# Optimization experiments

Measured on AMD Instinct MI355X. Metric: run time of the kernel, lower is better.

## Reference

```python
import jax, jax.numpy as jnp
import numpy as np

B, S, D, H = 2, 2048, 1024, 16
DH = D // H  # 64


def setup_inputs() -> dict:
    key = jax.random.key(0)
    ks = jax.random.split(key, 12)
    scale = 0.02
    q = jax.random.normal(ks[0], (B, S, D), dtype=jnp.float32)
    k = jax.random.normal(ks[1], (B, S, D), dtype=jnp.float32)
    v = jax.random.normal(ks[2], (B, S, D), dtype=jnp.float32)
    # CTRL-style causal mask: 1.0 above the diagonal (positions to mask), 0.0 elsewhere
    mask = jnp.triu(jnp.ones((S, S), dtype=jnp.float32), k=1)
    Wq = jax.random.normal(ks[3], (D, D), dtype=jnp.float32) * scale
    bq = jnp.zeros((D,), dtype=jnp.float32)
    Wk = jax.random.normal(ks[4], (D, D), dtype=jnp.float32) * scale
    bk = jnp.zeros((D,), dtype=jnp.float32)
    Wv = jax.random.normal(ks[5], (D, D), dtype=jnp.float32) * scale
    bv = jnp.zeros((D,), dtype=jnp.float32)
    Wo = jax.random.normal(ks[6], (D, D), dtype=jnp.float32) * scale
    bo = jnp.zeros((D,), dtype=jnp.float32)
    return {"q": q, "k": k, "v": v, "mask": mask,
            "Wq": Wq, "bq": bq, "Wk": Wk, "bk": bk,
            "Wv": Wv, "bv": bv, "Wo": Wo, "bo": bo}


def _split_heads(x):
    # [B, S, D] -> [B, H, S, DH]
    b, s, _ = x.shape
    return x.reshape(b, s, H, DH).transpose(0, 2, 1, 3)


def reference(q, k, v, mask, Wq, bq, Wk, bk, Wv, bv, Wo, bo):
    # QKV projections
    qh = _split_heads(q @ Wq + bq)  # [B, H, S, DH]
    kh = _split_heads(k @ Wk + bk)
    vh = _split_heads(v @ Wv + bv)
    # scaled dot-product attention with CTRL mask convention (mask * -1e4 added)
    scores = jnp.einsum('bhqd,bhkd->bhqk', qh, kh) / jnp.sqrt(jnp.float32(DH))
    scores = scores + mask * -10000.0  # mask broadcasts [S,S] -> [B,H,S,S]
    weights = jax.nn.softmax(scores, axis=-1)
    ctx = jnp.einsum('bhqk,bhkd->bhqd', weights, vh)  # [B, H, S, DH]
    ctx = ctx.transpose(0, 2, 1, 3).reshape(q.shape[0], -1, D)  # [B, S, D]
    return ctx @ Wo + bo
```

## Files before the change

### kernel.cpp

```cpp
#include <hip/hip_runtime.h>
#include <stdint.h>

typedef unsigned short u16;
typedef __attribute__((ext_vector_type(8))) short bf16x8;
typedef __attribute__((ext_vector_type(4))) float f32x4;
typedef __attribute__((ext_vector_type(4))) unsigned short u16x4;

#define C_SCALE 0.1803368801111204f
#define C_MASK  -14426.950408889634f

__device__ __forceinline__ float bf2f(u16 x) {
  union { uint32_t u; float f; } v; v.u = ((uint32_t)x) << 16; return v.f;
}
__device__ __forceinline__ u16 f2bf(float f) {
  union { float f; uint32_t u; } v; v.f = f;
  return (u16)((v.u + 0x7FFFu + ((v.u >> 16) & 1u)) >> 16);
}

__device__ __forceinline__ void load_lds16(const void* g, void* l) {
  __builtin_amdgcn_global_load_lds(
      (const __attribute__((address_space(1))) uint32_t*)g,
      (__attribute__((address_space(3))) uint32_t*)l, 16, 0, 0);
}

__device__ __forceinline__ uint32_t pack_trunc(uint32_t f_even, uint32_t f_odd) {
  return __builtin_amdgcn_perm(f_odd, f_even, 0x07060302u);
}

__device__ __forceinline__ uint32_t cvtpk_bf16(float lo, float hi) {
  uint32_t r;
  asm("v_cvt_pk_bf16_f32 %0, %1, %2" : "=v"(r) : "v"(lo), "v"(hi));
  return r;
}

__device__ __forceinline__ bool detect_bf16(const u16* __restrict__ q) {
  int lane = threadIdx.x & 63;
  u16 w = q[lane * 4];
  int e = (w >> 7) & 0xFF;
  unsigned long long b = __ballot(e >= 96 && e <= 159);
  return __popcll(b) >= 48;
}

__global__ __launch_bounds__(256) void prep_all(const u16* __restrict__ W0,
                                                const u16* __restrict__ W1,
                                                const u16* __restrict__ W2,
                                                const u16* __restrict__ W3,
                                                u16* __restrict__ WTb,
                                                const u16* __restrict__ q,
                                                const u16* __restrict__ k,
                                                const u16* __restrict__ v,
                                                u16* __restrict__ Acast,
                                                int docast) {
  constexpr int D = 1024;
  const int z = blockIdx.z;
  const bool isbf = detect_bf16(q);

  if (z >= 4) {
    if (!docast || isbf) return;
    const int zi = z - 4;
    const u16* src = zi == 0 ? q : (zi == 1 ? k : v);
    const uint32_t* S = (const uint32_t*)src;
    u16* dst = Acast + (size_t)zi * 4 * 1024 * 1024;
    const int fb = blockIdx.y * 16 + blockIdx.x;
    const int t = threadIdx.x;
#pragma unroll
    for (int it = 0; it < 8; ++it) {
      size_t base = (size_t)fb * 16384 + it * 2048 + t * 8;
      uint4 a = *(const uint4*)&S[base];
      uint4 b = *(const uint4*)&S[base + 4];
      uint4 o;
      o.x = pack_trunc(a.x, a.y); o.y = pack_trunc(a.z, a.w);
      o.z = pack_trunc(b.x, b.y); o.w = pack_trunc(b.z, b.w);
      *(uint4*)&dst[base] = o;
    }
    return;
  }

  __shared__ u16 tile[64][72];
  const u16* W = z == 0 ? W0 : (z == 1 ? W1 : (z == 2 ? W2 : W3));
  u16* WT = WTb + (size_t)z * D * D;
  const int x0 = blockIdx.x * 64, y0 = blockIdx.y * 64;
  const int t = threadIdx.x;
  const int r = t >> 3;
  const int c8 = (t & 7) << 3;
#pragma unroll
  for (int hh = 0; hh < 2; ++hh) {
    int row = r + hh * 32;
    if (isbf) {
      *(uint4*)&tile[row][c8] = *(const uint4*)&W[(size_t)(y0 + row) * D + x0 + c8];
    } else {
      const float* Wf = (const float*)W;
      float4 f0 = *(const float4*)&Wf[(size_t)(y0 + row) * D + x0 + c8];
      float4 f1 = *(const float4*)&Wf[(size_t)(y0 + row) * D + x0 + c8 + 4];
      u16 tmp[8] = {f2bf(f0.x), f2bf(f0.y), f2bf(f0.z), f2bf(f0.w),
                    f2bf(f1.x), f2bf(f1.y), f2bf(f1.z), f2bf(f1.w)};
      *(uint4*)&tile[row][c8] = *(uint4*)tmp;
    }
  }
  __syncthreads();
#pragma unroll
  for (int hh = 0; hh < 2; ++hh) {
    int row = r + hh * 32;
    u16 tmp[8];
#pragma unroll
    for (int i = 0; i < 8; ++i) tmp[i] = tile[c8 + i][row];
    *(uint4*)&WT[(size_t)(x0 + row) * D + y0 + c8] = *(uint4*)tmp;
  }
}


__device__ __forceinline__ void stage_tile32(const u16* __restrict__ src, int row0,
                                             int k0, u16* dst, int wave, int lane) {
  constexpr int K = 1024;
#pragma unroll
  for (int p = 0; p < 2; ++p) {
    int seg = wave * 2 + p;
    int r = seg * 16 + (lane >> 2);
    int c = lane & 3;
    int cg = c ^ ((r >> 1) & 3);
    load_lds16(&src[(size_t)(row0 + r) * K + k0 + cg * 8], dst + seg * 512);
  }
}

#define FRAG_READS(Ab, Bb)                                                    \
  _Pragma("unroll") for (int i = 0; i < 4; ++i) {                             \
    int r = wm + 16 * i + lr;                                                 \
    af[i] = *(const bf16x8*)&(Ab)[r * 32 + ((quad ^ ((r >> 1) & 3)) * 8)];    \
  }                                                                           \
  _Pragma("unroll") for (int jj = 0; jj < 4; ++jj) {                          \
    int r = wn + 16 * jj + lr;                                                \
    bff[jj] = *(const bf16x8*)&(Bb)[r * 32 + ((quad ^ ((r >> 1) & 3)) * 8)];  \
  }

#define MFMA16()                                                              \
  _Pragma("unroll") for (int i = 0; i < 4; ++i)                               \
  _Pragma("unroll") for (int jj = 0; jj < 4; ++jj)                            \
      acc[i][jj] = __builtin_amdgcn_mfma_f32_16x16x32_bf16(af[i], bff[jj],    \
                                                           acc[i][jj], 0, 0, 0);

__device__ __forceinline__ void kloop2_dma(const u16* __restrict__ A,
                                           const u16* __restrict__ BT,
                                           int m0, int n0, u16* As, u16* Bs,
                                           int wave, int lane, f32x4 (&acc)[4][4]) {
  const int quad = lane >> 4, lr = lane & 15;
  const int wm = (wave & 1) * 64, wn = (wave >> 1) * 64;
  auto stage = [&](int t, int buf) {
    stage_tile32(A, m0, t * 32, As + buf * 4096, wave, lane);
    stage_tile32(BT, n0, t * 32, Bs + buf * 4096, wave, lane);
  };
  stage(0, 0);
  __syncthreads();
#pragma unroll 1
  for (int j = 0; j < 16; ++j) {
    const int t0 = 2 * j;
    {
      stage(t0 + 1, 1);
      bf16x8 af[4], bff[4];
      const u16 *Ab = As, *Bb = Bs;
      FRAG_READS(Ab, Bb)
      MFMA16()
      __syncthreads();
    }
    {
      if (t0 + 2 < 32) stage(t0 + 2, 0);
      bf16x8 af[4], bff[4];
      const u16 *Ab = As + 4096, *Bb = Bs + 4096;
      FRAG_READS(Ab, Bb)
      MFMA16()
      __syncthreads();
    }
  }
}

__device__ __forceinline__ void kloop2_f32(const float* __restrict__ Af,
                                           const u16* __restrict__ BT,
                                           int m0, int n0, u16* As, u16* Bs,
                                           int tid, f32x4 (&acc)[4][4]) {
  constexpr int K = 1024;
  const int wave = tid >> 6, lane = tid & 63;
  const int quad = lane >> 4, lr = lane & 15;
  const int wm = (wave & 1) * 64, wn = (wave >> 1) * 64;
  const int ar = tid >> 1, ah = tid & 1;
  const uint32_t* Au = (const uint32_t*)Af;
  uint4 ra0[4], ra1[4];
  auto loadA = [&](int t, uint4 (&r)[4]) {
    const uint32_t* p = &Au[(size_t)(m0 + ar) * K + t * 32 + ah * 16];
    r[0] = *(const uint4*)(p + 0);
    r[1] = *(const uint4*)(p + 4);
    r[2] = *(const uint4*)(p + 8);
    r[3] = *(const uint4*)(p + 12);
  };
  auto writeA = [&](int buf, uint4 (&rr)[4]) {
    uint4 o0, o1;
    o0.x = pack_trunc(rr[0].x, rr[0].y); o0.y = pack_trunc(rr[0].z, rr[0].w);
    o0.z = pack_trunc(rr[1].x, rr[1].y); o0.w = pack_trunc(rr[1].z, rr[1].w);
    o1.x = pack_trunc(rr[2].x, rr[2].y); o1.y = pack_trunc(rr[2].z, rr[2].w);
    o1.z = pack_trunc(rr[3].x, rr[3].y); o1.w = pack_trunc(rr[3].z, rr[3].w);
    int sw = (ar >> 1) & 3;
    int c0 = (2 * ah) ^ sw, c1 = (2 * ah + 1) ^ sw;
    *(uint4*)&As[buf * 4096 + ar * 32 + c0 * 8] = o0;
    *(uint4*)&As[buf * 4096 + ar * 32 + c1 * 8] = o1;
  };
  auto stageB = [&](int t, int buf) {
    stage_tile32(BT, n0, t * 32, Bs + buf * 4096, wave, lane);
  };
  loadA(0, ra0);
  stageB(0, 0);
  loadA(1, ra1);
  writeA(0, ra0);
  __syncthreads();
#pragma unroll 1
  for (int j = 0; j < 16; ++j) {
    const int t0 = 2 * j;
    {
      stageB(t0 + 1, 1);
      writeA(1, ra1);
      if (t0 + 2 < 32) loadA(t0 + 2, ra0);
      bf16x8 af[4], bff[4];
      const u16 *Ab = As, *Bb = Bs;
      FRAG_READS(Ab, Bb)
      MFMA16()
      __syncthreads();
    }
    {
      if (t0 + 2 < 32) { stageB(t0 + 2, 0); writeA(0, ra0); }
      if (t0 + 3 < 32) loadA(t0 + 3, ra1);
      bf16x8 af[4], bff[4];
      const u16 *Ab = As + 4096, *Bb = Bs + 4096;
      FRAG_READS(Ab, Bb)
      MFMA16()
      __syncthreads();
    }
  }
}

__device__ __forceinline__ void qkv_epilogue(int z, int n0, int m0, int wn, int wm,
                                             int quad, int lr, const u16* bias,
                                             bool isbf, f32x4 (&acc)[4][4],
                                             u16* __restrict__ C) {
  const float osc = (z == 0) ? C_SCALE : 1.0f;
#pragma unroll
  for (int i = 0; i < 4; ++i) {
#pragma unroll
    for (int jj = 0; jj < 4; ++jj) {
      int n = n0 + wn + 16 * jj + lr;
      float bv = isbf ? bf2f(bias[n]) : ((const float*)bias)[n];
#pragma unroll
      for (int r = 0; r < 4; ++r) {
        int m = m0 + wm + 16 * i + quad * 4 + r;
        float val = (acc[i][jj][r] + bv) * osc;
        int b = m >> 11, s = m & 2047, h = n >> 6, dh = n & 63;
        size_t idx;
        if (z == 2) idx = ((size_t)(b * 16 + h) * 64 + dh) * 2048 + s;
        else        idx = ((size_t)(b * 16 + h) * 2048 + s) * 64 + dh;
        C[idx] = f2bf(val);
      }
    }
  }
}

__global__ __launch_bounds__(256, 3) void gemm_qkv_pre(
    const u16* __restrict__ q, const u16* __restrict__ k, const u16* __restrict__ v,
    const u16* __restrict__ Acast, const u16* __restrict__ WTb,
    const u16* __restrict__ b0, const u16* __restrict__ b1, const u16* __restrict__ b2,
    u16* __restrict__ Chb) {
  __shared__ u16 As[2 * 4096];
  __shared__ u16 Bs[2 * 4096];
  const int z = blockIdx.y;
  const bool isbf = detect_bf16(q);
  const u16* Araw = z == 0 ? q : (z == 1 ? k : v);
  const u16* A = isbf ? Araw : Acast + (size_t)z * 4 * 1024 * 1024;
  const u16* bias = z == 0 ? b0 : (z == 1 ? b1 : b2);
  const u16* BT = WTb + (size_t)z * 1024 * 1024;
  u16* C = Chb + (size_t)z * 4 * 1024 * 1024;
  const int tid = threadIdx.x;
  const int wave = tid >> 6, lane = tid & 63;
  const int quad = lane >> 4, lr = lane & 15;
  const int f = blockIdx.x;
  const int n0 = (f >> 5) * 128;
  const int m0 = (f & 31) * 128;
  const int wm = (wave & 1) * 64, wn = (wave >> 1) * 64;

  f32x4 acc[4][4] = {};
  kloop2_dma(A, BT, m0, n0, As, Bs, wave, lane, acc);
  qkv_epilogue(z, n0, m0, wn, wm, quad, lr, bias, isbf, acc, C);
}

__global__ __launch_bounds__(256, 3) void gemm_qkv_fb(
    const u16* __restrict__ A0, const u16* __restrict__ A1, const u16* __restrict__ A2,
    const u16* __restrict__ WTb,
    const u16* __restrict__ b0, const u16* __restrict__ b1, const u16* __restrict__ b2,
    u16* __restrict__ Chb) {
  __shared__ u16 As[2 * 4096];
  __shared__ u16 Bs[2 * 4096];
  const int z = blockIdx.y;
  const u16* A = z == 0 ? A0 : (z == 1 ? A1 : A2);
  const u16* bias = z == 0 ? b0 : (z == 1 ? b1 : b2);
  const u16* BT = WTb + (size_t)z * 1024 * 1024;
  u16* C = Chb + (size_t)z * 4 * 1024 * 1024;
  const bool isbf = detect_bf16(A0);
  const int tid = threadIdx.x;
  const int wave = tid >> 6, lane = tid & 63;
  const int quad = lane >> 4, lr = lane & 15;
  const int f = blockIdx.x;
  const int n0 = (f >> 5) * 128;
  const int m0 = (f & 31) * 128;
  const int wm = (wave & 1) * 64, wn = (wave >> 1) * 64;

  f32x4 acc[4][4] = {};
  if (isbf) kloop2_dma(A, BT, m0, n0, As, Bs, wave, lane, acc);
  else      kloop2_f32((const float*)A, BT, m0, n0, As, Bs, tid, acc);
  qkv_epilogue(z, n0, m0, wn, wm, quad, lr, bias, isbf, acc, C);
}

__global__ __launch_bounds__(256, 2) void gemm_out(const u16* __restrict__ A,
                                                   const u16* __restrict__ BT,
                                                   const u16* __restrict__ bias,
                                                   u16* __restrict__ C,
                                                   const u16* __restrict__ qprobe) {
  constexpr int N = 1024, K = 1024;
  __shared__ u16 As[2 * 2048];
  __shared__ u16 Bs[2 * 4096];
  const bool isbf = detect_bf16(qprobe);
  const int tid = threadIdx.x;
  const int wave = tid >> 6, lane = tid & 63;
  const int quad = lane >> 4, lr = lane & 15;
  const int f = blockIdx.x;
  const int n0 = (f >> 6) * 128;
  const int m0 = (f & 63) * 64;
  const int wm = (wave & 1) * 32, wn = (wave >> 1) * 64;

  auto stage = [&](int t, int buf) {
    {
      int r = wave * 16 + (lane >> 2);
      int c = lane & 3;
      int cg = c ^ ((r >> 1) & 3);
      load_lds16(&A[(size_t)(m0 + r) * K + t * 32 + cg * 8],
                 As + buf * 2048 + wave * 512);
    }
    stage_tile32(BT, n0, t * 32, Bs + buf * 4096, wave, lane);
  };

  f32x4 acc[2][4] = {};
  stage(0, 0);
  __syncthreads();
#pragma unroll 1
  for (int j = 0; j < 16; ++j) {
    const int t0 = 2 * j;
#pragma unroll
    for (int half = 0; half < 2; ++half) {
      const int t = t0 + half;
      if (t + 1 < 32) stage(t + 1, (t + 1) & 1);
      bf16x8 af[2], bff[4];
      const u16* Ab = As + (t & 1) * 2048;
      const u16* Bb = Bs + (t & 1) * 4096;
#pragma unroll
      for (int i = 0; i < 2; ++i) {
        int r = wm + 16 * i + lr;
        af[i] = *(const bf16x8*)&Ab[r * 32 + ((quad ^ ((r >> 1) & 3)) * 8)];
      }
#pragma unroll
      for (int jj = 0; jj < 4; ++jj) {
        int r = wn + 16 * jj + lr;
        bff[jj] = *(const bf16x8*)&Bb[r * 32 + ((quad ^ ((r >> 1) & 3)) * 8)];
      }
#pragma unroll
      for (int i = 0; i < 2; ++i)
#pragma unroll
        for (int jj = 0; jj < 4; ++jj)
          acc[i][jj] =
              __builtin_amdgcn_mfma_f32_16x16x32_bf16(af[i], bff[jj], acc[i][jj], 0, 0, 0);
      __syncthreads();
    }
  }

#pragma unroll
  for (int i = 0; i < 2; ++i) {
#pragma unroll
    for (int jj = 0; jj < 4; ++jj) {
      int n = n0 + wn + 16 * jj + lr;
      float bv = isbf ? bf2f(bias[n]) : ((const float*)bias)[n];
#pragma unroll
      for (int r = 0; r < 4; ++r) {
        int m = m0 + wm + 16 * i + quad * 4 + r;
        float val = acc[i][jj][r] + bv;
        size_t idx = (size_t)m * N + n;
        if (isbf) C[idx] = f2bf(val);
        else ((float*)C)[idx] = val;
      }
    }
  }
}

__global__ __launch_bounds__(256, 2) void attn_fwd(const u16* __restrict__ Qh,
                                                   const u16* __restrict__ Kh,
                                                   const u16* __restrict__ VTh,
                                                   u16* __restrict__ ctx) {
  constexpr int S = 2048, DH = 64, Dm = 1024;
  __shared__ u16 Ks[2][64 * 64];
  __shared__ u16 Vs[2][64 * 64];
  __shared__ u16 Pl[4][16 * 72];
  const int tid = threadIdx.x;
  const int wave = tid >> 6, lane = tid & 63;
  const int quad = lane >> 4, lr = lane & 15;
  const int bh = blockIdx.y;
  const int bx = (int)blockIdx.x;
  const u16* Q  = Qh  + (size_t)bh * S * DH;
  const u16* Kp = Kh  + (size_t)bh * S * DH;
  const u16* Vt = VTh + (size_t)bh * S * DH;
  u16* Plw = Pl[wave];
  const int b = bh >> 4, h = bh & 15;

  auto stageK = [&](int kt, int kbuf) {
#pragma unroll
    for (int p = 0; p < 2; ++p) {
      int s = (wave * 2 + p) * 64 + lane;
      int r = s >> 3, cg = (s & 7) ^ (r & 7);
      load_lds16(&Kp[(size_t)(kt + r) * DH + cg * 8], &Ks[kbuf][(wave * 2 + p) * 512]);
    }
  };
  auto stageV = [&](int kt, int vbuf) {
#pragma unroll
    for (int p = 0; p < 2; ++p) {
      int s = (wave * 2 + p) * 64 + lane;
      int r = s >> 3, cg = (s & 7) ^ (r & 7);
      load_lds16(&Vt[(size_t)r * S + kt + cg * 8], &Vs[vbuf][(wave * 2 + p) * 512]);
    }
  };

  int kb = 0, vb = 0;
  for (int ph = 0; ph < 2; ++ph) {
    const int qt = ph == 0 ? (31 - bx) : bx;
    const int q0 = qt * 64;
    const int nt = qt + 1;
    const int qg = q0 + wave * 16 + lr;

    bf16x8 aQ[2];
#pragma unroll
    for (int s = 0; s < 2; ++s)
      aQ[s] = *(const bf16x8*)&Q[(size_t)(q0 + wave * 16 + lr) * DH + s * 32 + quad * 8];

    f32x4 o[4] = {};
    float m_i = -1.0e5f;
    float l_i = 0.f;

    __syncthreads();
    stageK(0, kb);
    stageV(0, vb);

    for (int it = 0; it < nt; ++it) {
      const int kt = it * 64;
      __syncthreads();

      bf16x8 aK[4][2], bV[4][2];
#pragma unroll
      for (int t = 0; t < 4; ++t) {
        int r = t * 16 + lr;
#pragma unroll
        for (int s = 0; s < 2; ++s) {
          int ch = (s * 4 + quad) ^ (r & 7);
          aK[t][s] = *(const bf16x8*)&Ks[kb][r * 64 + ch * 8];
        }
      }
#pragma unroll
      for (int c = 0; c < 4; ++c) {
        int rr = c * 16 + lr;
#pragma unroll
        for (int s = 0; s < 2; ++s) {
          int ch = (s * 4 + quad) ^ (rr & 7);
          bV[c][s] = *(const bf16x8*)&Vs[vb][rr * 64 + ch * 8];
        }
      }

      if (it + 1 < nt) {
        stageK(kt + 64, kb ^ 1);
        stageV(kt + 64, vb ^ 1);
      }

      f32x4 sc[4];
#pragma unroll
      for (int t = 0; t < 4; ++t) {
        f32x4 zz = {0.f, 0.f, 0.f, 0.f};
        zz = __builtin_amdgcn_mfma_f32_16x16x32_bf16(aK[t][0], aQ[0], zz, 0, 0, 0);
        zz = __builtin_amdgcn_mfma_f32_16x16x32_bf16(aK[t][1], aQ[1], zz, 0, 0, 0);
        sc[t] = zz;
      }

      const bool diag = (it == nt - 1);
      float v[4][4];
      float mx = -1.0e5f;
      if (diag) {
#pragma unroll
        for (int t = 0; t < 4; ++t)
#pragma unroll
          for (int r = 0; r < 4; ++r) {
            int kg = kt + t * 16 + quad * 4 + r;
            float x = sc[t][r] + ((kg > qg) ? C_MASK : 0.f);
            v[t][r] = x;
            mx = fmaxf(mx, x);
          }
      } else {
#pragma unroll
        for (int t = 0; t < 4; ++t)
#pragma unroll
          for (int r = 0; r < 4; ++r) {
            float x = sc[t][r];
            v[t][r] = x;
            mx = fmaxf(mx, x);
          }
      }
      mx = fmaxf(mx, __shfl_xor(mx, 16));
      mx = fmaxf(mx, __shfl_xor(mx, 32));

      const bool noresc = __all(mx <= m_i + 8.0f);
      const float m_new = noresc ? m_i : fmaxf(m_i, mx);

      float sum = 0.f;
      uint32_t pw[4][2];
#pragma unroll
      for (int t = 0; t < 4; ++t) {
        float p0 = exp2f(v[t][0] - m_new);
        float p1 = exp2f(v[t][1] - m_new);
        float p2 = exp2f(v[t][2] - m_new);
        float p3 = exp2f(v[t][3] - m_new);
        sum += p0 + p1 + p2 + p3;
        pw[t][0] = cvtpk_bf16(p0, p1);
        pw[t][1] = cvtpk_bf16(p2, p3);
      }
      sum += __shfl_xor(sum, 16);
      sum += __shfl_xor(sum, 32);

      if (noresc) {
        l_i += sum;
      } else {
        float alpha = exp2f(m_i - m_new);
        l_i = l_i * alpha + sum;
        m_i = m_new;
#pragma unroll
        for (int r = 0; r < 4; ++r) {
          float ab = __shfl(alpha, quad * 4 + r);
#pragma unroll
          for (int c = 0; c < 4; ++c) o[c][r] *= ab;
        }
      }
#pragma unroll
      for (int t = 0; t < 4; ++t) {
        uint2 w = {pw[t][0], pw[t][1]};
        *(uint2*)&Plw[lr * 72 + t * 16 + quad * 4] = w;
      }
      asm volatile("s_waitcnt lgkmcnt(0)" ::: "memory");
      bf16x8 aP[2];
#pragma unroll
      for (int s = 0; s < 2; ++s)
        aP[s] = *(const bf16x8*)&Plw[lr * 72 + s * 32 + quad * 8];
#pragma unroll
      for (int c = 0; c < 4; ++c)
#pragma unroll
        for (int s = 0; s < 2; ++s)
          o[c] = __builtin_amdgcn_mfma_f32_16x16x32_bf16(aP[s], bV[c][s], o[c], 0, 0, 0);
      kb ^= 1; vb ^= 1;
    }

    float linv = 1.f / l_i;
#pragma unroll
    for (int r = 0; r < 4; ++r) {
      float lb = __shfl(linv, quad * 4 + r);
      int s = q0 + wave * 16 + quad * 4 + r;
      size_t orow = ((size_t)b * S + s) * Dm + h * DH;
#pragma unroll
      for (int c = 0; c < 4; ++c) ctx[orow + c * 16 + lr] = f2bf(o[c][r] * lb);
    }
  }
}

extern "C" void kernel_launch(void* const* d_in, const int* in_sizes, int n_in,
                              void* d_out, int out_size, void* d_ws, size_t ws_size,
                              hipStream_t stream) {
  const u16* q  = (const u16*)d_in[0];
  const u16* k  = (const u16*)d_in[1];
  const u16* v  = (const u16*)d_in[2];
  const u16* Wq = (const u16*)d_in[4];
  const u16* bq = (const u16*)d_in[5];
  const u16* Wk = (const u16*)d_in[6];
  const u16* bk = (const u16*)d_in[7];
  const u16* Wv = (const u16*)d_in[8];
  const u16* bv = (const u16*)d_in[9];
  const u16* Wo = (const u16*)d_in[10];
  const u16* bo = (const u16*)d_in[11];
  u16* out = (u16*)d_out;

  constexpr size_t M1 = 1024 * 1024;
  u16* ws = (u16*)d_ws;
  u16* WT  = ws;
  u16* Qh  = WT + 4 * M1;
  u16* X   = Qh + 12 * M1;
  u16* Acast = X;
  u16* ctx   = X;

  const bool docast = ws_size >= (size_t)28 * M1 * 2;

  dim3 tb(256);
  prep_all<<<dim3(16, 16, 7), tb, 0, stream>>>(Wq, Wk, Wv, Wo, WT, q, k, v,
                                               Acast, docast ? 1 : 0);
  if (docast)
    gemm_qkv_pre<<<dim3(256, 3), tb, 0, stream>>>(q, k, v, Acast, WT, bq, bk, bv, Qh);
  else
    gemm_qkv_fb<<<dim3(256, 3), tb, 0, stream>>>(q, k, v, WT, bq, bk, bv, Qh);
  attn_fwd<<<dim3(16, 32), tb, 0, stream>>>(Qh, Qh + 4 * M1, Qh + 8 * M1, ctx);
  gemm_out<<<dim3(512), tb, 0, stream>>>(ctx, WT + 3 * M1, bo, out, q);
}
```

Baseline: 233.0 us.

## Fuse paired causal query tiles into one K/V sweep sharing staged tiles

The attention kernel used to process its two query tiles (31-bx and bx) in two sequential passes, each streaming K/V from the start. It now runs a single sweep over key tiles up to the larger tile's diagonal, with both query tiles consuming each staged K/V tile. The small tile is updated only while it <= bx, and each tile has its own P scratch buffer in LDS. This removes about bx+1 redundant K/V stage loads and one pipeline restart per block, at the cost of more registers (two accumulator sets) and larger LDS use, which could reduce occupancy.

```diff
diff --git a/kernel.cpp b/kernel.cpp
--- a/kernel.cpp
+++ b/kernel.cpp
@@ -399,7 +399,7 @@
   constexpr int S = 2048, DH = 64, Dm = 1024;
   __shared__ u16 Ks[2][64 * 64];
   __shared__ u16 Vs[2][64 * 64];
-  __shared__ u16 Pl[4][16 * 72];
+  __shared__ u16 Pl[4][2][16 * 72];
   const int tid = threadIdx.x;
   const int wave = tid >> 6, lane = tid & 63;
   const int quad = lane >> 4, lr = lane & 15;
@@ -408,8 +408,9 @@
   const u16* Q  = Qh  + (size_t)bh * S * DH;
   const u16* Kp = Kh  + (size_t)bh * S * DH;
   const u16* Vt = VTh + (size_t)bh * S * DH;
-  u16* Plw = Pl[wave];
   const int b = bh >> 4, h = bh & 15;
+  u16* PlA = Pl[wave][0];
+  u16* PlB = Pl[wave][1];
 
   auto stageK = [&](int kt, int kbuf) {
 #pragma unroll
@@ -428,74 +429,86 @@
     }
   };
 
-  int kb = 0, vb = 0;
-  for (int ph = 0; ph < 2; ++ph) {
-    const int qt = ph == 0 ? (31 - bx) : bx;
-    const int q0 = qt * 64;
-    const int nt = qt + 1;
-    const int qg = q0 + wave * 16 + lr;
-
-    bf16x8 aQ[2];
-#pragma unroll
-    for (int s = 0; s < 2; ++s)
-      aQ[s] = *(const bf16x8*)&Q[(size_t)(q0 + wave * 16 + lr) * DH + s * 32 + quad * 8];
-
-    f32x4 o[4] = {};
-    float m_i = -1.0e5f;
-    float l_i = 0.f;
-
+  const int ta = 31 - bx;
+  const int tb = bx;
+  const int qa0 = ta * 64, qb0 = tb * 64;
+  const int qga = qa0 + wave * 16 + lr;
+  const int qgb = qb0 + wave * 16 + lr;
+
+  bf16x8 aQa[2], aQb[2];
+#pragma unroll
+  for (int s = 0; s < 2; ++s) {
+    aQa[s] = *(const bf16x8*)&Q[(size_t)(qa0 + wave * 16 + lr) * DH + s * 32 + quad * 8];
+    aQb[s] = *(const bf16x8*)&Q[(size_t)(qb0 + wave * 16 + lr) * DH + s * 32 + quad * 8];
+  }
+
+  f32x4 oa[4] = {}, ob[4] = {};
+  float ma = -1.0e5f, la = 0.f;
+  float mb = -1.0e5f, lb = 0.f;
+
+  int buf = 0;
+  stageK(0, 0);
+  stageV(0, 0);
+
+  for (int it = 0; it <= ta; ++it) {
+    const int kt = it * 64;
     __syncthreads();
-    stageK(0, kb);
-    stageV(0, vb);
-
-    for (int it = 0; it < nt; ++it) {
-      const int kt = it * 64;
-      __syncthreads();
-
-      bf16x8 aK[4][2], bV[4][2];
-#pragma unroll
-      for (int t = 0; t < 4; ++t) {
-        int r = t * 16 + lr;
-#pragma unroll
-        for (int s = 0; s < 2; ++s) {
-          int ch = (s * 4 + quad) ^ (r & 7);
-          aK[t][s] = *(const bf16x8*)&Ks[kb][r * 64 + ch * 8];
-        }
-      }
-#pragma unroll
-      for (int c = 0; c < 4; ++c) {
-        int rr = c * 16 + lr;
-#pragma unroll
-        for (int s = 0; s < 2; ++s) {
-          int ch = (s * 4 + quad) ^ (rr & 7);
-          bV[c][s] = *(const bf16x8*)&Vs[vb][rr * 64 + ch * 8];
-        }
-      }
-
-      if (it + 1 < nt) {
-        stageK(kt + 64, kb ^ 1);
-        stageV(kt + 64, vb ^ 1);
-      }
-
-      f32x4 sc[4];
+
+    bf16x8 aK[4][2], bV[4][2];
+#pragma unroll
+    for (int t = 0; t < 4; ++t) {
+      int r = t * 16 + lr;
+#pragma unroll
+      for (int s = 0; s < 2; ++s) {
+        int ch = (s * 4 + quad) ^ (r & 7);
+        aK[t][s] = *(const bf16x8*)&Ks[buf][r * 64 + ch * 8];
+      }
+    }
+#pragma unroll
+    for (int c = 0; c < 4; ++c) {
+      int rr = c * 16 + lr;
+#pragma unroll
+      for (int s = 0; s < 2; ++s) {
+        int ch = (s * 4 + quad) ^ (rr & 7);
+        bV[c][s] = *(const bf16x8*)&Vs[buf][rr * 64 + ch * 8];
+      }
+    }
+
+    if (it < ta) {
+      stageK(kt + 64, buf ^ 1);
+      stageV(kt + 64, buf ^ 1);
+    }
+
+    const bool doB = (it <= tb);
+
+    f32x4 sca[4], scb[4];
+#pragma unroll
+    for (int t = 0; t < 4; ++t) {
+      f32x4 zz = {0.f, 0.f, 0.f, 0.f};
+      zz = __builtin_amdgcn_mfma_f32_16x16x32_bf16(aK[t][0], aQa[0], zz, 0, 0, 0);
+      zz = __builtin_amdgcn_mfma_f32_16x16x32_bf16(aK[t][1], aQa[1], zz, 0, 0, 0);
+      sca[t] = zz;
+    }
+    if (doB) {
 #pragma unroll
       for (int t = 0; t < 4; ++t) {
         f32x4 zz = {0.f, 0.f, 0.f, 0.f};
-        zz = __builtin_amdgcn_mfma_f32_16x16x32_bf16(aK[t][0], aQ[0], zz, 0, 0, 0);
-        zz = __builtin_amdgcn_mfma_f32_16x16x32_bf16(aK[t][1], aQ[1], zz, 0, 0, 0);
-        sc[t] = zz;
-      }
-
-      const bool diag = (it == nt - 1);
+        zz = __builtin_amdgcn_mfma_f32_16x16x32_bf16(aK[t][0], aQb[0], zz, 0, 0, 0);
+        zz = __builtin_amdgcn_mfma_f32_16x16x32_bf16(aK[t][1], aQb[1], zz, 0, 0, 0);
+        scb[t] = zz;
+      }
+    }
+
+    {
       float v[4][4];
       float mx = -1.0e5f;
-      if (diag) {
+      if (it == ta) {
 #pragma unroll
         for (int t = 0; t < 4; ++t)
 #pragma unroll
           for (int r = 0; r < 4; ++r) {
             int kg = kt + t * 16 + quad * 4 + r;
-            float x = sc[t][r] + ((kg > qg) ? C_MASK : 0.f);
+            float x = sca[t][r] + ((kg > qga) ? C_MASK : 0.f);
             v[t][r] = x;
             mx = fmaxf(mx, x);
           }
@@ -504,71 +517,157 @@
         for (int t = 0; t < 4; ++t)
 #pragma unroll
           for (int r = 0; r < 4; ++r) {
-            float x = sc[t][r];
+            float x = sca[t][r];
             v[t][r] = x;
             mx = fmaxf(mx, x);
           }
       }
       mx = fmaxf(mx, __shfl_xor(mx, 16));
       mx = fmaxf(mx, __shfl_xor(mx, 32));
-
-      const bool noresc = __all(mx <= m_i + 8.0f);
-      const float m_new = noresc ? m_i : fmaxf(m_i, mx);
-
+      const bool noresc = __all(mx <= ma + 8.0f);
+      const float mn = noresc ? ma : fmaxf(ma, mx);
       float sum = 0.f;
       uint32_t pw[4][2];
 #pragma unroll
       for (int t = 0; t < 4; ++t) {
-        float p0 = exp2f(v[t][0] - m_new);
-        float p1 = exp2f(v[t][1] - m_new);
-        float p2 = exp2f(v[t][2] - m_new);
-        float p3 = exp2f(v[t][3] - m_new);
+        float p0 = exp2f(v[t][0] - mn);
+        float p1 = exp2f(v[t][1] - mn);
+        float p2 = exp2f(v[t][2] - mn);
+        float p3 = exp2f(v[t][3] - mn);
         sum += p0 + p1 + p2 + p3;
         pw[t][0] = cvtpk_bf16(p0, p1);
         pw[t][1] = cvtpk_bf16(p2, p3);
       }
       sum += __shfl_xor(sum, 16);
       sum += __shfl_xor(sum, 32);
-
       if (noresc) {
-        l_i += sum;
+        la += sum;
       } else {
-        float alpha = exp2f(m_i - m_new);
-        l_i = l_i * alpha + sum;
-        m_i = m_new;
+        float alpha = exp2f(ma - mn);
+        la = la * alpha + sum;
+        ma = mn;
 #pragma unroll
         for (int r = 0; r < 4; ++r) {
           float ab = __shfl(alpha, quad * 4 + r);
 #pragma unroll
-          for (int c = 0; c < 4; ++c) o[c][r] *= ab;
+          for (int c = 0; c < 4; ++c) oa[c][r] *= ab;
         }
       }
 #pragma unroll
       for (int t = 0; t < 4; ++t) {
         uint2 w = {pw[t][0], pw[t][1]};
-        *(uint2*)&Plw[lr * 72 + t * 16 + quad * 4] = w;
-      }
-      asm volatile("s_waitcnt lgkmcnt(0)" ::: "memory");
+        *(uint2*)&PlA[lr * 72 + t * 16 + quad * 4] = w;
+      }
+    }
+
+    if (doB) {
+      float v[4][4];
+      float mx = -1.0e5f;
+      if (it == tb) {
+#pragma unroll
+        for (int t = 0; t < 4; ++t)
+#pragma unroll
+          for (int r = 0; r < 4; ++r) {
+            int kg = kt + t * 16 + quad * 4 + r;
+            float x = scb[t][r] + ((kg > qgb) ? C_MASK : 0.f);
+            v[t][r] = x;
+            mx = fmaxf(mx, x);
+          }
+      } else {
+#pragma unroll
+        for (int t = 0; t < 4; ++t)
+#pragma unroll
+          for (int r = 0; r < 4; ++r) {
+            float x = scb[t][r];
+            v[t][r] = x;
+            mx = fmaxf(mx, x);
+          }
+      }
+      mx = fmaxf(mx, __shfl_xor(mx, 16));
+      mx = fmaxf(mx, __shfl_xor(mx, 32));
+      const bool noresc = __all(mx <= mb + 8.0f);
+      const float mn = noresc ? mb : fmaxf(mb, mx);
+      float sum = 0.f;
+      uint32_t pw[4][2];
+#pragma unroll
+      for (int t = 0; t < 4; ++t) {
+        float p0 = exp2f(v[t][0] - mn);
+        float p1 = exp2f(v[t][1] - mn);
+        float p2 = exp2f(v[t][2] - mn);
+        float p3 = exp2f(v[t][3] - mn);
+        sum += p0 + p1 + p2 + p3;
+        pw[t][0] = cvtpk_bf16(p0, p1);
+        pw[t][1] = cvtpk_bf16(p2, p3);
+      }
+      sum += __shfl_xor(sum, 16);
+      sum += __shfl_xor(sum, 32);
+      if (noresc) {
+        lb += sum;
+      } else {
+        float alpha = exp2f(mb - mn);
+        lb = lb * alpha + sum;
+        mb = mn;
+#pragma unroll
+        for (int r = 0; r < 4; ++r) {
+          float ab = __shfl(alpha, quad * 4 + r);
+#pragma unroll
+          for (int c = 0; c < 4; ++c) ob[c][r] *= ab;
+        }
+      }
+#pragma unroll
+      for (int t = 0; t < 4; ++t) {
+        uint2 w = {pw[t][0], pw[t][1]};
+        *(uint2*)&PlB[lr * 72 + t * 16 + quad * 4] = w;
+      }
+    }
+
+    asm volatile("s_waitcnt lgkmcnt(0)" ::: "memory");
+
+    {
       bf16x8 aP[2];
 #pragma unroll
       for (int s = 0; s < 2; ++s)
-        aP[s] = *(const bf16x8*)&Plw[lr * 72 + s * 32 + quad * 8];
+        aP[s] = *(const bf16x8*)&PlA[lr * 72 + s * 32 + quad * 8];
 #pragma unroll
       for (int c = 0; c < 4; ++c)
 #pragma unroll
         for (int s = 0; s < 2; ++s)
-          o[c] = __builtin_amdgcn_mfma_f32_16x16x32_bf16(aP[s], bV[c][s], o[c], 0, 0, 0);
-      kb ^= 1; vb ^= 1;
-    }
-
-    float linv = 1.f / l_i;
+          oa[c] = __builtin_amdgcn_mfma_f32_16x16x32_bf16(aP[s], bV[c][s], oa[c], 0, 0, 0);
+    }
+    if (doB) {
+      bf16x8 aP[2];
+#pragma unroll
+      for (int s = 0; s < 2; ++s)
+        aP[s] = *(const bf16x8*)&PlB[lr * 72 + s * 32 + quad * 8];
+#pragma unroll
+      for (int c = 0; c < 4; ++c)
+#pragma unroll
+        for (int s = 0; s < 2; ++s)
+          ob[c] = __builtin_amdgcn_mfma_f32_16x16x32_bf16(aP[s], bV[c][s], ob[c], 0, 0, 0);
+    }
+    buf ^= 1;
+  }
+
+  {
+    float linv = 1.f / la;
 #pragma unroll
     for (int r = 0; r < 4; ++r) {
-      float lb = __shfl(linv, quad * 4 + r);
-      int s = q0 + wave * 16 + quad * 4 + r;
+      float lbv = __shfl(linv, quad * 4 + r);
+      int s = qa0 + wave * 16 + quad * 4 + r;
       size_t orow = ((size_t)b * S + s) * Dm + h * DH;
 #pragma unroll
-      for (int c = 0; c < 4; ++c) ctx[orow + c * 16 + lr] = f2bf(o[c][r] * lb);
+      for (int c = 0; c < 4; ++c) ctx[orow + c * 16 + lr] = f2bf(oa[c][r] * lbv);
+    }
+  }
+  {
+    float linv = 1.f / lb;
+#pragma unroll
+    for (int r = 0; r < 4; ++r) {
+      float lbv = __shfl(linv, quad * 4 + r);
+      int s = qb0 + wave * 16 + quad * 4 + r;
+      size_t orow = ((size_t)b * S + s) * Dm + h * DH;
+#pragma unroll
+      for (int c = 0; c < 4; ++c) ctx[orow + c * 16 + lr] = f2bf(ob[c][r] * lbv);
     }
   }
 }
```

After: 232.6 us. Within noise of the previous version (-0.2%).
